# Performance work log

Measured on AMD Instinct MI355X. Metric: run time of the kernel, lower is better.

Reference implementation:

```python
import jax, jax.numpy as jnp
import numpy as np
from jax import lax

# Fixed dims from MSSMamba defaults
B_, L_, DM = 2, 8192, 256
NH, HP, NS = 4, 64, 8          # nheads, headdim, d_state
DIN = NH * HP                  # d_inner = 256
DPROJ = 2 * DIN + 2 * NS + NH  # 532


def setup_inputs() -> dict:
    key = jax.random.key(0)
    ks = jax.random.split(key, 16)
    f = lambda k, s, sc=1.0: jax.random.normal(k, s, jnp.float32) * sc
    inp = {
        'x_H': f(ks[0], (B_, L_, DM)),
        'x_V': f(ks[1], (B_, L_, DM)),
        'W_in_H': f(ks[2], (DM, 2 * DPROJ), 0.05),
        'W_in_V': f(ks[3], (DM, 2 * DPROJ), 0.05),
        'W_out_HF': f(ks[4], (DIN, DM), 0.05),
        'W_out_HB': f(ks[5], (DIN, DM), 0.05),
        'W_out_VF': f(ks[6], (DIN, DM), 0.05),
        'W_out_VB': f(ks[7], (DIN, DM), 0.05),
        'W_out': f(ks[8], (4 * DM, DM), 0.05),
    }
    for i, nm in enumerate(['HF', 'HB', 'VF', 'VB']):
        kd = jax.random.fold_in(ks[9], i)
        ka = jax.random.fold_in(ks[10], i)
        inp['dt_bias_' + nm] = f(kd, (NH,), 0.1)
        inp['A_log_' + nm] = jnp.log(jax.random.uniform(ka, (NH,), jnp.float32, 1.0, 16.0))
        inp['D_' + nm] = jnp.ones((NH,), jnp.float32)
    # per-batch permutation mapping vertical position -> horizontal position
    inp['v2h'] = jax.vmap(lambda k: jax.random.permutation(k, L_))(
        jax.random.split(ks[11], B_)).astype(jnp.int32)
    return inp


def _scan_dir(zxbcdt, dt_bias, A_log, D):
    # zxbcdt: [b, l, DPROJ] -> Mamba2-style selective scan, ngroups=1
    z = zxbcdt[..., :DIN].reshape(B_, L_, NH, HP)
    xBC = jax.nn.silu(zxbcdt[..., DIN:DIN + DIN + 2 * NS])
    x = xBC[..., :DIN].reshape(B_, L_, NH, HP)
    Bm = xBC[..., DIN:DIN + NS]      # [b, l, n]
    Cm = xBC[..., DIN + NS:]         # [b, l, n]
    dt = jax.nn.softplus(zxbcdt[..., -NH:] + dt_bias)  # [b, l, h]
    A = -jnp.exp(A_log)              # [h]
    dA = jnp.exp(dt * A)             # [b, l, h]
    dBx = jnp.einsum('blh,bln,blhp->blhpn', dt, Bm, x)  # [b,l,h,p,n]

    def step(state, inp):
        dA_t, dBx_t, C_t = inp
        state = dA_t[..., None, None] * state + dBx_t   # [b,h,p,n]
        y_t = jnp.einsum('bhpn,bn->bhp', state, C_t)
        return state, y_t

    init = jnp.zeros((B_, NH, HP, NS), dt.dtype)
    _, ys = lax.scan(step, init, (jnp.moveaxis(dA, 1, 0),
                                  jnp.moveaxis(dBx, 1, 0),
                                  jnp.moveaxis(Cm, 1, 0)))
    y = jnp.moveaxis(ys, 0, 1) + D[None, None, :, None] * x  # skip D*x
    y = y * jax.nn.silu(z)                                   # gate
    return y.reshape(B_, L_, DIN)


def reference(x_H, x_V, W_in_H, W_in_V,
              dt_bias_HF, dt_bias_HB, dt_bias_VF, dt_bias_VB,
              A_log_HF, A_log_HB, A_log_VF, A_log_VB,
              D_HF, D_HB, D_VF, D_VB,
              W_out_HF, W_out_HB, W_out_VF, W_out_VB,
              W_out, v2h):
    zx_HF, zx_HB = jnp.split(x_H @ W_in_H, 2, axis=-1)
    zx_VF, zx_VB = jnp.split(x_V @ W_in_V, 2, axis=-1)
    # note: source applies out_proj_HB to the HF branch (kept faithful)
    y_HF = _scan_dir(zx_HF, dt_bias_HF, A_log_HF, D_HF) @ W_out_HB
    y_HB = _scan_dir(zx_HB[:, ::-1], dt_bias_HB, A_log_HB, D_HB)[:, ::-1] @ W_out_HF
    y_VF = _scan_dir(zx_VF, dt_bias_VF, A_log_VF, D_VF) @ W_out_VB
    y_VB = _scan_dir(zx_VB[:, ::-1], dt_bias_VB, A_log_VB, D_VB)[:, ::-1] @ W_out_VF
    # remap vertical-ordered outputs to horizontal ordering (scatter by v2h)
    bidx = jnp.arange(B_)[:, None]
    y_VF = jnp.zeros_like(y_VF).at[bidx, v2h].set(y_VF)
    y_VB = jnp.zeros_like(y_VB).at[bidx, v2h].set(y_VB)
    cat = jnp.concatenate([y_HF, y_HB, y_VF, y_VB], axis=-1)  # [b, l, 4*d_model]
    return jax.nn.silu(cat) @ W_out
```

## Files before the change

### kernel.cpp

```cpp
#include <hip/hip_runtime.h>
#include <hip/hip_bf16.h>

#define B_N 2
#define L_N 8192
#define ROWS 16384
#define CHUNK 64
#define NCHUNK 128
#define GRP 16
#define NGRP 8
#define NPAD 1152

typedef __bf16 bf16x8 __attribute__((ext_vector_type(8)));
typedef float f32x4 __attribute__((ext_vector_type(4)));

__device__ __forceinline__ float siluf(float v) {
  return v * __builtin_amdgcn_rcpf(1.f + __expf(-v));
}
__device__ __forceinline__ float softplusf_(float v) {
  return fmaxf(v, 0.f) + log1pf(__expf(-fabsf(v)));
}
__device__ __forceinline__ unsigned short f2bf(float v) {
  union { __bf16 b; unsigned short u; } x;
  x.b = (__bf16)v;
  return x.u;
}
__device__ __forceinline__ float bf2f(unsigned short u) {
  union { unsigned u; float f; } x; x.u = ((unsigned)u) << 16;
  return x.f;
}

__device__ __forceinline__ void gload_lds16(const unsigned short* g, unsigned short* l) {
  __builtin_amdgcn_global_load_lds(
      (const __attribute__((address_space(1))) unsigned int*)g,
      (__attribute__((address_space(3))) unsigned int*)l, 16, 0, 0);
}

struct P4 { const float* p[4]; };
struct ScanConsts {
  const float* dt_bias[4];
  const float* A_log[4];
  const float* D[4];
};

__global__ __launch_bounds__(256) void k_prep(
    const float* __restrict__ xH, const float* __restrict__ xV,
    const float* __restrict__ WH, const float* __restrict__ WV,
    P4 ws, const float* __restrict__ W_out, const int* __restrict__ v2h, ScanConsts sc,
    unsigned short* __restrict__ xbf, float* __restrict__ dtv_arr, float* __restrict__ dA_arr,
    unsigned short* __restrict__ Wt_in, unsigned short* __restrict__ Wt_dirs,
    unsigned short* __restrict__ Wt_fin, int* __restrict__ inv) {
  __shared__ float xs[32][257];
  __shared__ float Wsm[8][260];
  int bid = blockIdx.x;
  int tid = threadIdx.x;
  if (bid < 1024) {
    const int mat = bid >> 9;
    const float* x = mat ? xV : xH;
    const float* W = mat ? WV : WH;
    const int r0 = (bid & 511) * 32;
    for (int i = tid; i < 2048; i += 256) {
      int c = i >> 8, k = i & 255;
      int sl = c >> 2, h = c & 3;
      Wsm[c][k] = W[(long)k * 1064 + sl * 532 + 528 + h];
    }
    for (int i = tid; i < 32 * 64; i += 256) {
      int rl = i >> 6, kq = (i & 63) * 4;
      float4 v = *(const float4*)(x + (long)(r0 + rl) * 256 + kq);
      xs[rl][kq + 0] = v.x; xs[rl][kq + 1] = v.y; xs[rl][kq + 2] = v.z; xs[rl][kq + 3] = v.w;
    }
    __syncthreads();
    for (int i = tid; i < 32 * 64; i += 256) {
      int rl = i >> 6, kq = (i & 63) * 4;
      ushort4 o;
      o.x = f2bf(xs[rl][kq + 0]);
      o.y = f2bf(xs[rl][kq + 1]);
      o.z = f2bf(xs[rl][kq + 2]);
      o.w = f2bf(xs[rl][kq + 3]);
      *(ushort4*)(xbf + (size_t)mat * ROWS * 256 + (long)(r0 + rl) * 256 + kq) = o;
    }
    const int rl = tid >> 3, c = tid & 7;
    float s = 0.f;
    #pragma unroll 8
    for (int k = 0; k < 256; ++k) s = fmaf(xs[rl][k], Wsm[c][k], s);
    const int sl = c >> 2, h = c & 3;
    const int dir = mat * 2 + sl;
    float dtv = softplusf_(s + sc.dt_bias[dir][h]);
    float dAv = __expf(dtv * (-__expf(sc.A_log[dir][h])));
    long o = ((long)dir * 4 + h) * ROWS + (r0 + rl);
    dtv_arr[o] = dtv;
    dA_arr[o] = dAv;
  } else if (bid < 3328) {
    int i = (bid - 1024) * 256 + tid;
    int z = i / (NPAD * 256);
    int rem = i - z * (NPAD * 256);
    int n = rem >> 8, k = rem & 255;
    const float* W = z ? WV : WH;
    int sl = n >= 544;
    int cc = n - (sl ? 544 : 0);
    float v = (cc < 532) ? W[(long)k * 1064 + sl * 532 + cc] : 0.f;
    Wt_in[i] = f2bf(v);
  } else if (bid < 4352) {
    int i = (bid - 3328) * 256 + tid;
    int d = i >> 16;
    int rem = i & 65535;
    int n = rem >> 8, k = rem & 255;
    Wt_dirs[i] = f2bf(ws.p[d][(long)k * 256 + n]);
  } else if (bid < 5376) {
    int i = (bid - 4352) * 256 + tid;
    int n = i >> 10, k = i & 1023;
    Wt_fin[i] = f2bf(W_out[(long)k * 256 + n]);
  } else {
    int m = (bid - 5376) * 256 + tid;
    if (m < ROWS) {
      int b = m >> 13;
      inv[b * L_N + v2h[m]] = m;
    }
  }
}

struct EpiIn {
  unsigned short* zraw;
  unsigned short* xraw;
  unsigned short* bc;
};

__global__ __launch_bounds__(256) void k_gemm_in(
    const unsigned short* __restrict__ Abase, const unsigned short* __restrict__ Btbase,
    EpiIn ep) {
  __shared__ unsigned short smem[24576];
  const int tid = threadIdx.x;
  const int lane = tid & 63;
  const int wid = tid >> 6;
  const int wm = wid & 1, wn = wid >> 1;
  const int q = lane >> 4, r = lane & 15;
  const int hbid = blockIdx.x;
  const int xcd = hbid & 7;
  const int j = hbid >> 3;
  const int m0 = (xcd * 16 + (j & 15)) * 128;
  const int n0 = ((j >> 4) % 9) * 128;
  const int z = j / 144;
  const unsigned short* A = Abase + (long)z * ROWS * 256;
  const unsigned short* Bt = Btbase + (long)z * NPAD * 256;

  int s_row[2], s_ch[2];
  #pragma unroll
  for (int i = 0; i < 2; ++i) {
    int idx = i * 256 + tid;
    s_row[i] = idx >> 2;
    s_ch[i] = (idx & 3) ^ ((s_row[i] >> 1) & 3);
  }

  auto stage = [&](int ti) {
    const int slot = ti % 3;
    const int kt = ti * 32;
    #pragma unroll
    for (int i = 0; i < 2; ++i) {
      gload_lds16(A + (long)(m0 + s_row[i]) * 256 + kt + s_ch[i] * 8,
                  smem + (size_t)slot * 4096 + (size_t)(i * 256 + wid * 64) * 8);
      gload_lds16(Bt + (long)(n0 + s_row[i]) * 256 + kt + s_ch[i] * 8,
                  smem + 12288 + (size_t)slot * 4096 + (size_t)(i * 256 + wid * 64) * 8);
    }
  };

  f32x4 acc[4][4] = {};
  const int swr = (r >> 1) & 3;

  stage(0);
  stage(1);

  #pragma unroll
  for (int i = 0; i < 8; ++i) {
    if (i < 7) asm volatile("s_waitcnt vmcnt(4)" ::: "memory");
    else       asm volatile("s_waitcnt vmcnt(0)" ::: "memory");
    __builtin_amdgcn_s_barrier();
    __builtin_amdgcn_sched_barrier(0);
    if (i + 2 < 8) stage(i + 2);
    const int slot = i % 3;
    bf16x8 af[4], bfr[4];
    #pragma unroll
    for (int mi = 0; mi < 4; ++mi)
      af[mi] = *(const bf16x8*)&smem[(size_t)slot * 4096 +
                                     ((wm * 64 + mi * 16 + r) * 4 + (q ^ swr)) * 8];
    #pragma unroll
    for (int ni = 0; ni < 4; ++ni)
      bfr[ni] = *(const bf16x8*)&smem[12288 + (size_t)slot * 4096 +
                                      ((wn * 64 + ni * 16 + r) * 4 + (q ^ swr)) * 8];
    __builtin_amdgcn_s_setprio(1);
    #pragma unroll
    for (int mi = 0; mi < 4; ++mi)
      #pragma unroll
      for (int ni = 0; ni < 4; ++ni)
        acc[mi][ni] = __builtin_amdgcn_mfma_f32_16x16x32_bf16(af[mi], bfr[ni], acc[mi][ni], 0, 0, 0);
    __builtin_amdgcn_s_setprio(0);
  }
  __syncthreads();

  unsigned short* tr = smem + wid * (16 * 72);
  #pragma unroll
  for (int mi = 0; mi < 4; ++mi) {
    #pragma unroll
    for (int ni = 0; ni < 4; ++ni)
      #pragma unroll
      for (int j2 = 0; j2 < 4; ++j2)
        tr[(q * 4 + j2) * 72 + ni * 16 + r] = f2bf(acc[mi][ni][j2]);
    asm volatile("s_waitcnt lgkmcnt(0)" ::: "memory");
    #pragma unroll
    for (int pass = 0; pass < 2; ++pass) {
      int rl = pass * 8 + (lane >> 3);
      int c8 = (lane & 7) * 8;
      bf16x8 v = *(const bf16x8*)&tr[rl * 72 + c8];
      int row = m0 + wm * 64 + mi * 16 + rl;
      int col = n0 + wn * 64 + c8;
      int sl = col >= 544;
      int cc = col - (sl ? 544 : 0);
      if (cc < 528) {
        int dir = z * 2 + sl;
        if (cc < 256)
          *(bf16x8*)(ep.zraw + ((long)dir * ROWS + row) * 256 + cc) = v;
        else if (cc < 512)
          *(bf16x8*)(ep.xraw + ((long)dir * ROWS + row) * 256 + cc - 256) = v;
        else
          *(bf16x8*)(ep.bc + ((long)dir * ROWS + row) * 16 + cc - 512) = v;
      }
    }
    asm volatile("s_waitcnt lgkmcnt(0)" ::: "memory");
  }
}

__global__ __launch_bounds__(1024) void k_fuse(
    const unsigned short* __restrict__ ybf,
    const unsigned short* __restrict__ Wt_dirs,
    const unsigned short* __restrict__ Wt_fin,
    const int* __restrict__ inv,
    float* __restrict__ out) {
  __shared__ unsigned short smf[47616];
  unsigned short* Ab = smf;
  unsigned short* Bb = smf + 6144;
  unsigned short* Tl = smf + 30720;
  float* Ttmp = (float*)(smf + 30720);
  const int tid = threadIdx.x;
  const int lane = tid & 63;
  const int wid = tid >> 6;
  const int wm = wid & 3, wn = wid >> 2;
  const int q = lane >> 4, r = lane & 15;
  const int r0 = blockIdx.x * 64;
  const int swr = (r >> 1) & 3;
  const bool wA = (wid < 4);

  const int a_row = tid >> 2;
  const int a_ch = (tid & 3) ^ ((a_row >> 1) & 3);
  const long a_offH = (long)(r0 + a_row) * 256 + a_ch * 8;
  long a_offV = 0;
  if (tid < 256) a_offV = (long)inv[r0 + a_row] * 256 + a_ch * 8;
  const int b_row = tid >> 2;
  const int b_ch = (tid & 3) ^ ((b_row >> 1) & 3);

  auto stageT = [&](int g) {
    const int seg = g >> 3, ti = g & 7, kt = ti * 32;
    const int dl = seg >> 1;
    const int slot = g % 3;
    if ((seg & 1) == 0) {
      const long aoff = (dl >= 2) ? a_offV : a_offH;
      if (tid < 256)
        gload_lds16(ybf + (long)dl * ROWS * 256 + aoff + kt,
                    Ab + (size_t)slot * 2048 + (size_t)(wid * 64) * 8);
      gload_lds16(Wt_dirs + (long)dl * 65536 + (long)b_row * 256 + kt + b_ch * 8,
                  Bb + (size_t)slot * 8192 + (size_t)(wid * 64) * 8);
    } else {
      gload_lds16(Wt_fin + (long)b_row * 1024 + dl * 256 + kt + b_ch * 8,
                  Bb + (size_t)slot * 8192 + (size_t)(wid * 64) * 8);
    }
  };

  f32x4 acc_o[4] = {};

  stageT(0);
  stageT(1);

  #pragma unroll
  for (int d = 0; d < 4; ++d) {
    f32x4 acc_t[4] = {};
    #pragma unroll
    for (int i = 0; i < 8; ++i) {
      const int g = d * 16 + i;
      if (wA) {
        if (i < 7) asm volatile("s_waitcnt vmcnt(2)" ::: "memory");
        else       asm volatile("s_waitcnt vmcnt(1)" ::: "memory");
      } else {
        asm volatile("s_waitcnt vmcnt(1)" ::: "memory");
      }
      __builtin_amdgcn_s_barrier();
      __builtin_amdgcn_sched_barrier(0);
      stageT(g + 2);
      const int slot = g % 3;
      bf16x8 af, bfr[4];
      af = *(const bf16x8*)&Ab[(size_t)slot * 2048 +
                               ((wm * 16 + r) * 4 + (q ^ swr)) * 8];
      #pragma unroll
      for (int ni = 0; ni < 4; ++ni)
        bfr[ni] = *(const bf16x8*)&Bb[(size_t)slot * 8192 +
                                      ((wn * 64 + ni * 16 + r) * 4 + (q ^ swr)) * 8];
      __builtin_amdgcn_s_setprio(1);
      #pragma unroll
      for (int ni = 0; ni < 4; ++ni)
        acc_t[ni] = __builtin_amdgcn_mfma_f32_16x16x32_bf16(af, bfr[ni], acc_t[ni], 0, 0, 0);
      __builtin_amdgcn_s_setprio(0);
    }
    #pragma unroll
    for (int ni = 0; ni < 4; ++ni)
      #pragma unroll
      for (int jj = 0; jj < 4; ++jj)
        Tl[(wm * 16 + q * 4 + jj) * 264 + wn * 64 + ni * 16 + r] =
            f2bf(siluf(acc_t[ni][jj]));
    asm volatile("s_waitcnt lgkmcnt(0)" ::: "memory");
    #pragma unroll
    for (int i = 0; i < 8; ++i) {
      const int g = d * 16 + 8 + i;
      if (g == 63) {
        asm volatile("s_waitcnt vmcnt(0)" ::: "memory");
      } else if (wA && i == 7) {
        asm volatile("s_waitcnt vmcnt(2)" ::: "memory");
      } else {
        asm volatile("s_waitcnt vmcnt(1)" ::: "memory");
      }
      __builtin_amdgcn_s_barrier();
      __builtin_amdgcn_sched_barrier(0);
      if (g + 2 < 64) stageT(g + 2);
      const int slot = g % 3;
      const int kt = i * 32;
      bf16x8 af, bfr[4];
      af = *(const bf16x8*)&Tl[(wm * 16 + r) * 264 + kt + q * 8];
      #pragma unroll
      for (int ni = 0; ni < 4; ++ni)
        bfr[ni] = *(const bf16x8*)&Bb[(size_t)slot * 8192 +
                                      ((wn * 64 + ni * 16 + r) * 4 + (q ^ swr)) * 8];
      __builtin_amdgcn_s_setprio(1);
      #pragma unroll
      for (int ni = 0; ni < 4; ++ni)
        acc_o[ni] = __builtin_amdgcn_mfma_f32_16x16x32_bf16(af, bfr[ni], acc_o[ni], 0, 0, 0);
      __builtin_amdgcn_s_setprio(0);
    }
  }

  __syncthreads();
  #pragma unroll
  for (int h = 0; h < 2; ++h) {
    if ((wm >> 1) == h) {
      #pragma unroll
      for (int ni = 0; ni < 4; ++ni)
        #pragma unroll
        for (int jj = 0; jj < 4; ++jj)
          Ttmp[((wm & 1) * 16 + q * 4 + jj) * 260 + wn * 64 + ni * 16 + r] = acc_o[ni][jj];
    }
    __syncthreads();
    #pragma unroll
    for (int pass = 0; pass < 2; ++pass) {
      int id = pass * 1024 + tid;
      int row = id >> 6, c4 = (id & 63) * 4;
      float4 v = *(const float4*)&Ttmp[row * 260 + c4];
      *(float4*)(out + (long)(r0 + h * 32 + row) * 256 + c4) = v;
    }
    if (h == 0) __syncthreads();
  }
}

struct ScanP {
  const unsigned short* xraw;
  const unsigned short* zraw;
  const unsigned short* bc;
  const float* dtv;
  const float* dA;
  const float* D[4];
};

__global__ __launch_bounds__(512) void k_scan1(ScanP sp, float* __restrict__ S,
                                               float* __restrict__ P) {
  __shared__ __align__(16) float Bst[8][CHUNK][8];
  __shared__ float dAs[8][CHUNK];
  const int tid = threadIdx.x;
  const int p = tid & 63;
  const int w = tid >> 6;
  const int c = blockIdx.x;
  const int d = blockIdx.y;
  const int bh = w;
  const int b = bh >> 2, h = bh & 3;
  const int rev = d & 1;
  const int t0 = c * CHUNK;
  {
    const int t = t0 + p;
    const int l = rev ? (L_N - 1 - t) : t;
    const int row = (b << 13) + l;
    uint4 bv = *(const uint4*)(sp.bc + ((long)d * ROWS + row) * 16);
    const unsigned short* bu = (const unsigned short*)&bv;
    float dtvv = sp.dtv[((long)d * 4 + h) * ROWS + row];
    dAs[w][p] = sp.dA[((long)d * 4 + h) * ROWS + row];
    #pragma unroll
    for (int n = 0; n < 8; ++n) Bst[w][p][n] = siluf(bf2f(bu[n])) * dtvv;
  }
  __syncthreads();

  float st[8] = {0, 0, 0, 0, 0, 0, 0, 0};
  float cumdA = 1.f;
  const int l0 = rev ? (L_N - 1 - t0) : t0;
  const unsigned short* xp = sp.xraw + ((long)d * ROWS + (b << 13) + l0) * 256 + h * 64 + p;
  const long stp = rev ? -256L : 256L;

  unsigned short xa[4], xb[4];
  #pragma unroll
  for (int j = 0; j < 4; ++j) xa[j] = xp[(long)j * stp];
  #pragma unroll
  for (int g = 0; g < CHUNK / 4; ++g) {
    if (g < CHUNK / 4 - 1) {
      #pragma unroll
      for (int j = 0; j < 4; ++j) xb[j] = xp[(long)((g + 1) * 4 + j) * stp];
    }
    #pragma unroll
    for (int j = 0; j < 4; ++j) {
      int s = g * 4 + j;
      float x = siluf(bf2f(xa[j]));
      float dA = dAs[w][s];
      f32x4 B0 = *(const f32x4*)&Bst[w][s][0];
      f32x4 B1 = *(const f32x4*)&Bst[w][s][4];
      cumdA *= dA;
      st[0] = fmaf(dA, st[0], x * B0[0]);
      st[1] = fmaf(dA, st[1], x * B0[1]);
      st[2] = fmaf(dA, st[2], x * B0[2]);
      st[3] = fmaf(dA, st[3], x * B0[3]);
      st[4] = fmaf(dA, st[4], x * B1[0]);
      st[5] = fmaf(dA, st[5], x * B1[1]);
      st[6] = fmaf(dA, st[6], x * B1[2]);
      st[7] = fmaf(dA, st[7], x * B1[3]);
    }
    #pragma unroll
    for (int j = 0; j < 4; ++j) xa[j] = xb[j];
  }
  float* Sp = S + ((((long)d * NCHUNK + c) * 8 + bh) * 64 + p) * 8;
  #pragma unroll
  for (int n = 0; n < 8; ++n) Sp[n] = st[n];
  if (p == 0) P[((long)d * NCHUNK + c) * 8 + bh] = cumdA;
}

__global__ __launch_bounds__(512) void k_scan2a(const float* __restrict__ S,
                                                const float* __restrict__ P,
                                                float* __restrict__ carry_loc,
                                                float* __restrict__ Sg,
                                                float* __restrict__ Pg) {
  __shared__ float Pl[GRP];
  const int tid = threadIdx.x;
  const int gid = blockIdx.x;
  const int g = gid & (NGRP - 1);
  const int dbh = gid >> 3;
  const int d = dbh >> 3, bh = dbh & 7;
  if (tid < GRP) Pl[tid] = P[((long)d * NCHUNK + g * GRP + tid) * 8 + bh];
  __syncthreads();
  float cy = 0.f;
  #pragma unroll
  for (int i = 0; i < GRP; ++i) {
    const int c = g * GRP + i;
    carry_loc[(((long)d * NCHUNK + c) * 8 + bh) * 512 + tid] = cy;
    const float Sv = S[(((long)d * NCHUNK + c) * 8 + bh) * 512 + tid];
    cy = fmaf(Pl[i], cy, Sv);
  }
  Sg[(((long)d * NGRP + g) * 8 + bh) * 512 + tid] = cy;
  if (tid == 0) {
    float pp = 1.f;
    #pragma unroll
    for (int i = 0; i < GRP; ++i) pp *= Pl[i];
    Pg[((long)d * NGRP + g) * 8 + bh] = pp;
  }
}

__global__ __launch_bounds__(512) void k_scan2b(const float* __restrict__ Sg,
                                                const float* __restrict__ Pg,
                                                float* __restrict__ gcarry) {
  __shared__ float Pgl[NGRP];
  const int tid = threadIdx.x;
  const int dbh = blockIdx.x;
  const int d = dbh >> 3, bh = dbh & 7;
  if (tid < NGRP) Pgl[tid] = Pg[((long)d * NGRP + tid) * 8 + bh];
  __syncthreads();
  float cy = 0.f;
  #pragma unroll
  for (int g = 0; g < NGRP; ++g) {
    gcarry[(((long)d * NGRP + g) * 8 + bh) * 512 + tid] = cy;
    const float Sv = Sg[(((long)d * NGRP + g) * 8 + bh) * 512 + tid];
    cy = fmaf(Pgl[g], cy, Sv);
  }
}

__global__ __launch_bounds__(512) void k_scan3(ScanP sp,
                                               const float* __restrict__ carry_loc,
                                               const float* __restrict__ gcarry,
                                               const float* __restrict__ Pc,
                                               unsigned short* __restrict__ ybf) {
  __shared__ __align__(16) float Bst[8][CHUNK][8];
  __shared__ __align__(16) float Cst[8][CHUNK][8];
  __shared__ float dAs[8][CHUNK];
  __shared__ float Pgr[8][GRP];
  const int tid = threadIdx.x;
  const int p = tid & 63;
  const int w = tid >> 6;
  const int c = blockIdx.x;
  const int d = blockIdx.y;
  const int bh = w;
  const int b = bh >> 2, h = bh & 3;
  const int rev = d & 1;
  const float Dv = sp.D[d][h];
  const int t0 = c * CHUNK;
  const int grp = c >> 4, ii = c & 15;
  if (p < ii) Pgr[w][p] = Pc[((long)d * NCHUNK + grp * GRP + p) * 8 + bh];
  {
    const int t = t0 + p;
    const int l = rev ? (L_N - 1 - t) : t;
    const int row = (b << 13) + l;
    const unsigned short* bp = sp.bc + ((long)d * ROWS + row) * 16;
    uint4 bv = *(const uint4*)bp;
    uint4 cv = *(const uint4*)(bp + 8);
    const unsigned short* bu = (const unsigned short*)&bv;
    const unsigned short* cu = (const unsigned short*)&cv;
    float dtvv = sp.dtv[((long)d * 4 + h) * ROWS + row];
    dAs[w][p] = sp.dA[((long)d * 4 + h) * ROWS + row];
    #pragma unroll
    for (int n = 0; n < 8; ++n) Bst[w][p][n] = siluf(bf2f(bu[n])) * dtvv;
    #pragma unroll
    for (int n = 0; n < 8; ++n) Cst[w][p][n] = siluf(bf2f(cu[n]));
  }
  __syncthreads();

  float pref = 1.f;
  for (int k = 0; k < ii; ++k) pref *= Pgr[w][k];
  float st[8];
  {
    const float* clp = carry_loc + ((((long)d * NCHUNK + c) * 8 + bh) * 64 + p) * 8;
    const float* gcp = gcarry + ((((long)d * NGRP + grp) * 8 + bh) * 64 + p) * 8;
    #pragma unroll
    for (int n = 0; n < 8; ++n) st[n] = fmaf(pref, gcp[n], clp[n]);
  }

  const int l0 = rev ? (L_N - 1 - t0) : t0;
  const long base = (long)(b << 13) + l0;
  const unsigned short* xp = sp.xraw + ((long)d * ROWS + base) * 256 + h * 64 + p;
  const unsigned short* zp = sp.zraw + ((long)d * ROWS + base) * 256 + h * 64 + p;
  unsigned short* yp = ybf + ((long)d * ROWS + base) * 256 + h * 64 + p;
  const long stp = rev ? -256L : 256L;

  unsigned short xa[4], xb[4], za[4], zb[4];
  #pragma unroll
  for (int j = 0; j < 4; ++j) { xa[j] = xp[(long)j * stp]; za[j] = zp[(long)j * stp]; }
  #pragma unroll
  for (int g = 0; g < CHUNK / 4; ++g) {
    if (g < CHUNK / 4 - 1) {
      #pragma unroll
      for (int j = 0; j < 4; ++j) {
        xb[j] = xp[(long)((g + 1) * 4 + j) * stp];
        zb[j] = zp[(long)((g + 1) * 4 + j) * stp];
      }
    }
    #pragma unroll
    for (int j = 0; j < 4; ++j) {
      int s = g * 4 + j;
      float x = siluf(bf2f(xa[j]));
      float zv = siluf(bf2f(za[j]));
      float dA = dAs[w][s];
      f32x4 B0 = *(const f32x4*)&Bst[w][s][0];
      f32x4 B1 = *(const f32x4*)&Bst[w][s][4];
      f32x4 C0 = *(const f32x4*)&Cst[w][s][0];
      f32x4 C1 = *(const f32x4*)&Cst[w][s][4];
      st[0] = fmaf(dA, st[0], x * B0[0]);
      st[1] = fmaf(dA, st[1], x * B0[1]);
      st[2] = fmaf(dA, st[2], x * B0[2]);
      st[3] = fmaf(dA, st[3], x * B0[3]);
      st[4] = fmaf(dA, st[4], x * B1[0]);
      st[5] = fmaf(dA, st[5], x * B1[1]);
      st[6] = fmaf(dA, st[6], x * B1[2]);
      st[7] = fmaf(dA, st[7], x * B1[3]);
      float y01 = fmaf(st[1], C0[1], st[0] * C0[0]);
      float y23 = fmaf(st[3], C0[3], st[2] * C0[2]);
      float y45 = fmaf(st[5], C1[1], st[4] * C1[0]);
      float y67 = fmaf(st[7], C1[3], st[6] * C1[2]);
      float y = (y01 + y23) + (y45 + y67);
      y = fmaf(Dv, x, y) * zv;
      yp[(long)s * stp] = f2bf(y);
    }
    #pragma unroll
    for (int j = 0; j < 4; ++j) { xa[j] = xb[j]; za[j] = zb[j]; }
  }
}

extern "C" void kernel_launch(void* const* d_in, const int* in_sizes, int n_in,
                              void* d_out, int out_size, void* d_ws, size_t ws_size,
                              hipStream_t stream) {
  const float* x_H = (const float*)d_in[0];
  const float* x_V = (const float*)d_in[1];
  const float* W_in_H = (const float*)d_in[2];
  const float* W_in_V = (const float*)d_in[3];
  const float* W_out_HF = (const float*)d_in[4];
  const float* W_out_HB = (const float*)d_in[5];
  const float* W_out_VF = (const float*)d_in[6];
  const float* W_out_VB = (const float*)d_in[7];
  const float* W_out = (const float*)d_in[8];
  const float* dt_bias_HF = (const float*)d_in[9];
  const float* A_log_HF = (const float*)d_in[10];
  const float* D_HF = (const float*)d_in[11];
  const float* dt_bias_HB = (const float*)d_in[12];
  const float* A_log_HB = (const float*)d_in[13];
  const float* D_HB = (const float*)d_in[14];
  const float* dt_bias_VF = (const float*)d_in[15];
  const float* A_log_VF = (const float*)d_in[16];
  const float* D_VF = (const float*)d_in[17];
  const float* dt_bias_VB = (const float*)d_in[18];
  const float* A_log_VB = (const float*)d_in[19];
  const float* D_VB = (const float*)d_in[20];
  const int* v2h = (const int*)d_in[21];

  char* ws = (char*)d_ws;
  size_t off = 0;
  auto alloc = [&](size_t bytes) {
    void* pp = ws + off;
    off = (off + bytes + 255) & ~(size_t)255;
    return pp;
  };
  unsigned short* xbf = (unsigned short*)alloc((size_t)2 * ROWS * 256 * 2);
  unsigned short* Wt_in = (unsigned short*)alloc((size_t)2 * NPAD * 256 * 2);
  unsigned short* Wt_dirs = (unsigned short*)alloc((size_t)4 * 65536 * 2);
  unsigned short* Wt_fin = (unsigned short*)alloc((size_t)256 * 1024 * 2);
  unsigned short* zraw = (unsigned short*)alloc((size_t)4 * ROWS * 256 * 2);
  unsigned short* xraw = (unsigned short*)alloc((size_t)4 * ROWS * 256 * 2);
  unsigned short* bc = (unsigned short*)alloc((size_t)4 * ROWS * 16 * 2);
  float* dtv_arr = (float*)alloc((size_t)16 * ROWS * 4);
  float* dA_arr = (float*)alloc((size_t)16 * ROWS * 4);
  unsigned short* ybf = (unsigned short*)alloc((size_t)4 * ROWS * 256 * 2);
  float* S = (float*)alloc((size_t)4 * NCHUNK * 8 * 512 * 4);
  float* P = (float*)alloc((size_t)4 * NCHUNK * 8 * 4);
  float* carry_loc = (float*)alloc((size_t)4 * NCHUNK * 8 * 512 * 4);
  float* Sg = (float*)alloc((size_t)4 * NGRP * 8 * 512 * 4);
  float* Pg = (float*)alloc((size_t)4 * NGRP * 8 * 4);
  float* gcarry = (float*)alloc((size_t)4 * NGRP * 8 * 512 * 4);
  int* inv = (int*)alloc((size_t)ROWS * 4);

  ScanConsts sc;
  sc.dt_bias[0] = dt_bias_HF; sc.dt_bias[1] = dt_bias_HB;
  sc.dt_bias[2] = dt_bias_VF; sc.dt_bias[3] = dt_bias_VB;
  sc.A_log[0] = A_log_HF; sc.A_log[1] = A_log_HB;
  sc.A_log[2] = A_log_VF; sc.A_log[3] = A_log_VB;
  sc.D[0] = D_HF; sc.D[1] = D_HB; sc.D[2] = D_VF; sc.D[3] = D_VB;

  P4 wdirs;
  wdirs.p[0] = W_out_HB; wdirs.p[1] = W_out_HF; wdirs.p[2] = W_out_VB; wdirs.p[3] = W_out_VF;

  k_prep<<<5440, 256, 0, stream>>>(x_H, x_V, W_in_H, W_in_V, wdirs, W_out, v2h, sc,
                                   xbf, dtv_arr, dA_arr, Wt_in, Wt_dirs, Wt_fin, inv);

  EpiIn ep; ep.zraw = zraw; ep.xraw = xraw; ep.bc = bc;

  k_gemm_in<<<2304, 256, 0, stream>>>(xbf, Wt_in, ep);

  ScanP sp;
  sp.xraw = xraw; sp.zraw = zraw; sp.bc = bc; sp.dtv = dtv_arr; sp.dA = dA_arr;
  sp.D[0] = D_HF; sp.D[1] = D_HB; sp.D[2] = D_VF; sp.D[3] = D_VB;

  k_scan1<<<dim3(NCHUNK, 4), 512, 0, stream>>>(sp, S, P);
  k_scan2a<<<32 * NGRP, 512, 0, stream>>>(S, P, carry_loc, Sg, Pg);
  k_scan2b<<<32, 512, 0, stream>>>(Sg, Pg, gcarry);
  k_scan3<<<dim3(NCHUNK, 4), 512, 0, stream>>>(sp, carry_loc, gcarry, P, ybf);

  k_fuse<<<256, 1024, 0, stream>>>(ybf, Wt_dirs, Wt_fin, inv, (float*)d_out);

  (void)in_sizes; (void)n_in; (void)out_size; (void)ws_size;
}
```

Baseline: 233.7 us.

## Fold group-carry scan into scan3 and double waves in input GEMM

```diff
diff --git a/kernel.cpp b/kernel.cpp
--- a/kernel.cpp
+++ b/kernel.cpp
@@ -124,14 +124,14 @@
   unsigned short* bc;
 };
 
-__global__ __launch_bounds__(256) void k_gemm_in(
+__global__ __launch_bounds__(512) void k_gemm_in(
     const unsigned short* __restrict__ Abase, const unsigned short* __restrict__ Btbase,
     EpiIn ep) {
   __shared__ unsigned short smem[24576];
   const int tid = threadIdx.x;
   const int lane = tid & 63;
   const int wid = tid >> 6;
-  const int wm = wid & 1, wn = wid >> 1;
+  const int wm = wid & 3, wn = wid >> 2;
   const int q = lane >> 4, r = lane & 15;
   const int hbid = blockIdx.x;
   const int xcd = hbid & 7;
@@ -142,27 +142,19 @@
   const unsigned short* A = Abase + (long)z * ROWS * 256;
   const unsigned short* Bt = Btbase + (long)z * NPAD * 256;
 
-  int s_row[2], s_ch[2];
-  #pragma unroll
-  for (int i = 0; i < 2; ++i) {
-    int idx = i * 256 + tid;
-    s_row[i] = idx >> 2;
-    s_ch[i] = (idx & 3) ^ ((s_row[i] >> 1) & 3);
-  }
+  const int s_row = tid >> 2;
+  const int s_ch = (tid & 3) ^ ((s_row >> 1) & 3);
 
   auto stage = [&](int ti) {
     const int slot = ti % 3;
     const int kt = ti * 32;
-    #pragma unroll
-    for (int i = 0; i < 2; ++i) {
-      gload_lds16(A + (long)(m0 + s_row[i]) * 256 + kt + s_ch[i] * 8,
-                  smem + (size_t)slot * 4096 + (size_t)(i * 256 + wid * 64) * 8);
-      gload_lds16(Bt + (long)(n0 + s_row[i]) * 256 + kt + s_ch[i] * 8,
-                  smem + 12288 + (size_t)slot * 4096 + (size_t)(i * 256 + wid * 64) * 8);
-    }
+    gload_lds16(A + (long)(m0 + s_row) * 256 + kt + s_ch * 8,
+                smem + (size_t)slot * 4096 + (size_t)(wid * 64) * 8);
+    gload_lds16(Bt + (long)(n0 + s_row) * 256 + kt + s_ch * 8,
+                smem + 12288 + (size_t)slot * 4096 + (size_t)(wid * 64) * 8);
   };
 
-  f32x4 acc[4][4] = {};
+  f32x4 acc[2][4] = {};
   const int swr = (r >> 1) & 3;
 
   stage(0);
@@ -170,24 +162,24 @@
 
   #pragma unroll
   for (int i = 0; i < 8; ++i) {
-    if (i < 7) asm volatile("s_waitcnt vmcnt(4)" ::: "memory");
+    if (i < 7) asm volatile("s_waitcnt vmcnt(2)" ::: "memory");
     else       asm volatile("s_waitcnt vmcnt(0)" ::: "memory");
     __builtin_amdgcn_s_barrier();
     __builtin_amdgcn_sched_barrier(0);
     if (i + 2 < 8) stage(i + 2);
     const int slot = i % 3;
-    bf16x8 af[4], bfr[4];
-    #pragma unroll
-    for (int mi = 0; mi < 4; ++mi)
+    bf16x8 af[2], bfr[4];
+    #pragma unroll
+    for (int mi = 0; mi < 2; ++mi)
       af[mi] = *(const bf16x8*)&smem[(size_t)slot * 4096 +
-                                     ((wm * 64 + mi * 16 + r) * 4 + (q ^ swr)) * 8];
+                                     ((wm * 32 + mi * 16 + r) * 4 + (q ^ swr)) * 8];
     #pragma unroll
     for (int ni = 0; ni < 4; ++ni)
       bfr[ni] = *(const bf16x8*)&smem[12288 + (size_t)slot * 4096 +
                                       ((wn * 64 + ni * 16 + r) * 4 + (q ^ swr)) * 8];
     __builtin_amdgcn_s_setprio(1);
     #pragma unroll
-    for (int mi = 0; mi < 4; ++mi)
+    for (int mi = 0; mi < 2; ++mi)
       #pragma unroll
       for (int ni = 0; ni < 4; ++ni)
         acc[mi][ni] = __builtin_amdgcn_mfma_f32_16x16x32_bf16(af[mi], bfr[ni], acc[mi][ni], 0, 0, 0);
@@ -197,7 +189,7 @@
 
   unsigned short* tr = smem + wid * (16 * 72);
   #pragma unroll
-  for (int mi = 0; mi < 4; ++mi) {
+  for (int mi = 0; mi < 2; ++mi) {
     #pragma unroll
     for (int ni = 0; ni < 4; ++ni)
       #pragma unroll
@@ -209,7 +201,7 @@
       int rl = pass * 8 + (lane >> 3);
       int c8 = (lane & 7) * 8;
       bf16x8 v = *(const bf16x8*)&tr[rl * 72 + c8];
-      int row = m0 + wm * 64 + mi * 16 + rl;
+      int row = m0 + wm * 32 + mi * 16 + rl;
       int col = n0 + wn * 64 + c8;
       int sl = col >= 544;
       int cc = col - (sl ? 544 : 0);
@@ -470,27 +462,10 @@
   }
 }
 
-__global__ __launch_bounds__(512) void k_scan2b(const float* __restrict__ Sg,
-                                                const float* __restrict__ Pg,
-                                                float* __restrict__ gcarry) {
-  __shared__ float Pgl[NGRP];
-  const int tid = threadIdx.x;
-  const int dbh = blockIdx.x;
-  const int d = dbh >> 3, bh = dbh & 7;
-  if (tid < NGRP) Pgl[tid] = Pg[((long)d * NGRP + tid) * 8 + bh];
-  __syncthreads();
-  float cy = 0.f;
-  #pragma unroll
-  for (int g = 0; g < NGRP; ++g) {
-    gcarry[(((long)d * NGRP + g) * 8 + bh) * 512 + tid] = cy;
-    const float Sv = Sg[(((long)d * NGRP + g) * 8 + bh) * 512 + tid];
-    cy = fmaf(Pgl[g], cy, Sv);
-  }
-}
-
 __global__ __launch_bounds__(512) void k_scan3(ScanP sp,
                                                const float* __restrict__ carry_loc,
-                                               const float* __restrict__ gcarry,
+                                               const float* __restrict__ Sg,
+                                               const float* __restrict__ Pg,
                                                const float* __restrict__ Pc,
                                                unsigned short* __restrict__ ybf) {
   __shared__ __align__(16) float Bst[8][CHUNK][8];
@@ -527,14 +502,21 @@
   }
   __syncthreads();
 
+  float gc[8] = {0, 0, 0, 0, 0, 0, 0, 0};
+  for (int g = 0; g < grp; ++g) {
+    const float Pgv = Pg[((long)d * NGRP + g) * 8 + bh];
+    const float* Sgp = Sg + (((long)d * NGRP + g) * 8 + bh) * 512 + p * 8;
+    #pragma unroll
+    for (int n = 0; n < 8; ++n) gc[n] = fmaf(Pgv, gc[n], Sgp[n]);
+  }
+
   float pref = 1.f;
   for (int k = 0; k < ii; ++k) pref *= Pgr[w][k];
   float st[8];
   {
     const float* clp = carry_loc + ((((long)d * NCHUNK + c) * 8 + bh) * 64 + p) * 8;
-    const float* gcp = gcarry + ((((long)d * NGRP + grp) * 8 + bh) * 64 + p) * 8;
-    #pragma unroll
-    for (int n = 0; n < 8; ++n) st[n] = fmaf(pref, gcp[n], clp[n]);
+    #pragma unroll
+    for (int n = 0; n < 8; ++n) st[n] = fmaf(pref, gc[n], clp[n]);
   }
 
   const int l0 = rev ? (L_N - 1 - t0) : t0;
@@ -635,7 +617,6 @@
   float* carry_loc = (float*)alloc((size_t)4 * NCHUNK * 8 * 512 * 4);
   float* Sg = (float*)alloc((size_t)4 * NGRP * 8 * 512 * 4);
   float* Pg = (float*)alloc((size_t)4 * NGRP * 8 * 4);
-  float* gcarry = (float*)alloc((size_t)4 * NGRP * 8 * 512 * 4);
   int* inv = (int*)alloc((size_t)ROWS * 4);
 
   ScanConsts sc;
@@ -653,7 +634,7 @@
 
   EpiIn ep; ep.zraw = zraw; ep.xraw = xraw; ep.bc = bc;
 
-  k_gemm_in<<<2304, 256, 0, stream>>>(xbf, Wt_in, ep);
+  k_gemm_in<<<2304, 512, 0, stream>>>(xbf, Wt_in, ep);
 
   ScanP sp;
   sp.xraw = xraw; sp.zraw = zraw; sp.bc = bc; sp.dtv = dtv_arr; sp.dA = dA_arr;
@@ -661,8 +642,7 @@
 
   k_scan1<<<dim3(NCHUNK, 4), 512, 0, stream>>>(sp, S, P);
   k_scan2a<<<32 * NGRP, 512, 0, stream>>>(S, P, carry_loc, Sg, Pg);
-  k_scan2b<<<32, 512, 0, stream>>>(Sg, Pg, gcarry);
-  k_scan3<<<dim3(NCHUNK, 4), 512, 0, stream>>>(sp, carry_loc, gcarry, P, ybf);
+  k_scan3<<<dim3(NCHUNK, 4), 512, 0, stream>>>(sp, carry_loc, Sg, Pg, P, ybf);
 
   k_fuse<<<256, 1024, 0, stream>>>(ybf, Wt_dirs, Wt_fin, inv, (float*)d_out);
 
```

Measured after the change: 242.3 us. 1.04x slower.
